# Kernel tuning notes

Hardware: AMD Instinct MI355X
Metric: run time of the kernel (lower is better)

The kernel has to match this reference:

```python
import jax, jax.numpy as jnp
import numpy as np

N = 100_000   # nodes
E = 1_600_000 # edges
D = 128       # in_dim == hidden_dim
G = 256       # graphs in batch
X = 16        # extra_in_dim (descriptor)
L = 3         # num_layers
C = 1         # n_classes
LN_EPS = 1e-5

def layer_norm(x, gamma, beta):
    mu = jnp.mean(x, axis=-1, keepdims=True)
    var = jnp.mean(jnp.square(x - mu), axis=-1, keepdims=True)
    return (x - mu) * jax.lax.rsqrt(var + LN_EPS) * gamma + beta

def setup_inputs() -> dict:
    key = jax.random.key(0)
    ks = jax.random.split(key, 24)
    s = 0.05
    inp = {
        "h": jax.random.normal(ks[0], (N, D), dtype=jnp.float32),
        "desc": jax.random.normal(ks[1], (G, X), dtype=jnp.float32),
        "src": jax.random.randint(ks[2], (E,), 0, N, dtype=jnp.int32),
        "dst": jax.random.randint(ks[3], (E,), 0, N, dtype=jnp.int32),
        "gid": jnp.sort(jax.random.randint(ks[4], (N,), 0, G, dtype=jnp.int32)),
        # stacked per-layer GIN params (all layers D->D)
        "W1": jax.random.normal(ks[5], (L, D, D), dtype=jnp.float32) * s,
        "b1": jnp.zeros((L, D), dtype=jnp.float32),
        "g1": jnp.ones((L, D), dtype=jnp.float32),   # inner LN gamma
        "be1": jnp.zeros((L, D), dtype=jnp.float32),  # inner LN beta
        "W2": jax.random.normal(ks[6], (L, D, D), dtype=jnp.float32) * s,
        "b2": jnp.zeros((L, D), dtype=jnp.float32),
        "eps": jnp.zeros((L,), dtype=jnp.float32),    # learnable eps per layer
        "ng": jnp.ones((L, D), dtype=jnp.float32),    # outer LN gamma
        "nb": jnp.zeros((L, D), dtype=jnp.float32),   # outer LN beta
        "fc1W": jax.random.normal(ks[7], (D + X, D), dtype=jnp.float32) * s,
        "fc1b": jnp.zeros((D,), dtype=jnp.float32),
        "n1g": jnp.ones((D,), dtype=jnp.float32),
        "n1b": jnp.zeros((D,), dtype=jnp.float32),
        "fc2W": jax.random.normal(ks[8], (D, C), dtype=jnp.float32) * s,
        "fc2b": jnp.zeros((C,), dtype=jnp.float32),
    }
    return inp

def reference(h, desc, src, dst, gid, W1, b1, g1, be1, W2, b2, eps, ng, nb,
              fc1W, fc1b, n1g, n1b, fc2W, fc2b):
    for l in range(L):
        # GIN aggregation: (1+eps)*h_v + sum_{u in N(v)} h_u
        agg = jax.ops.segment_sum(h[src], dst, num_segments=N)  # [N, D]
        x = (1.0 + eps[l]) * h + agg
        # apply_func MLP: Linear -> LN -> ReLU -> (Dropout=id) -> Linear
        x = jax.nn.relu(layer_norm(x @ W1[l] + b1[l], g1[l], be1[l]))
        x = x @ W2[l] + b2[l]
        # outer norm + relu (dropout = identity at eval)
        h = jax.nn.relu(layer_norm(x, ng[l], nb[l]))
    hg = jax.ops.segment_sum(h, gid, num_segments=G)  # sum pooling [G, D]
    x = jnp.concatenate([hg, desc], axis=1)           # [G, D+X]
    x = jax.nn.relu(layer_norm(x @ fc1W + fc1b, n1g, n1b))
    return x @ fc2W + fc2b                            # [G, C]
```

## Files before the change

### kernel.cpp

```cpp
#include <hip/hip_runtime.h>

#define NN 100000
#define NE 1600000
#define DD 128
#define NG 256
#define XX 16
#define NL 3
#define NBK 391
#define LNEPS 1e-5f

typedef _Float16 half8 __attribute__((ext_vector_type(8)));
typedef _Float16 half4v __attribute__((ext_vector_type(4)));
typedef float f32x4 __attribute__((ext_vector_type(4)));

__global__ __launch_bounds__(256) void hist_k(const int* __restrict__ dst,
                                              int* __restrict__ hist) {
    __shared__ int lh[NBK];
    const int t = threadIdx.x, blk = blockIdx.x;
    for (int i = t; i < NBK; i += 256) lh[i] = 0;
    __syncthreads();
    const int base = blk * (NE / 256);
    for (int e = base + t; e < base + NE / 256; e += 256)
        atomicAdd(&lh[dst[e] >> 8], 1);
    __syncthreads();
    for (int i = t; i < NBK; i += 256) hist[i * 256 + blk] = lh[i];
}

__global__ __launch_bounds__(256) void bucketpref_k(int* __restrict__ hist,
                                                    int* __restrict__ btot) {
    __shared__ int sd[256];
    const int b = blockIdx.x, t = threadIdx.x;
    int v = hist[b * 256 + t];
    sd[t] = v;
    __syncthreads();
    #pragma unroll
    for (int off = 1; off < 256; off <<= 1) {
        int x = t >= off ? sd[t - off] : 0;
        __syncthreads();
        sd[t] += x;
        __syncthreads();
    }
    hist[b * 256 + t] = sd[t] - v;
    if (t == 255) btot[b] = sd[255];
}

__global__ __launch_bounds__(512) void scan_bsums2_k(int* __restrict__ bsum, int nb,
                                                     int* __restrict__ row_ptr) {
    __shared__ int sd[512];
    int t = threadIdx.x;
    int v = t < nb ? bsum[t] : 0;
    sd[t] = v;
    __syncthreads();
    #pragma unroll
    for (int off = 1; off < 512; off <<= 1) {
        int x = t >= off ? sd[t - off] : 0;
        __syncthreads();
        sd[t] += x;
        __syncthreads();
    }
    if (t < nb) bsum[t] = sd[t] - v;
    if (t == 0) row_ptr[NN] = NE;
}

__global__ __launch_bounds__(256) void scatter_pairs_k(const int* __restrict__ src,
                                                       const int* __restrict__ dst,
                                                       const int* __restrict__ btot,
                                                       const int* __restrict__ hist,
                                                       unsigned* __restrict__ pairs) {
    __shared__ int off[NBK];
    const int t = threadIdx.x, blk = blockIdx.x;
    for (int i = t; i < NBK; i += 256)
        off[i] = btot[i] + hist[i * 256 + blk];
    __syncthreads();
    const int base = blk * (NE / 256);
    for (int e = base + t; e < base + NE / 256; e += 256) {
        int d = dst[e];
        int pos = atomicAdd(&off[d >> 8], 1);
        pairs[pos] = ((unsigned)(d & 255) << 17) | (unsigned)src[e];
    }
}

__global__ __launch_bounds__(256) void bucket_csr_k(const unsigned* __restrict__ pairs,
                                                    const int* __restrict__ btot,
                                                    int* __restrict__ row_ptr,
                                                    int* __restrict__ col) {
    __shared__ int cntL[256], ex[256], rnk[256], sd[256];
    const int b = blockIdx.x, t = threadIdx.x;
    const int nbase = b << 8;
    const int ps = btot[b];
    const int pe = (b == NBK - 1) ? NE : btot[b + 1];
    cntL[t] = 0; rnk[t] = 0;
    __syncthreads();
    for (int i = ps + t; i < pe; i += 256)
        atomicAdd(&cntL[pairs[i] >> 17], 1);
    __syncthreads();
    int v = cntL[t];
    sd[t] = v;
    __syncthreads();
    #pragma unroll
    for (int off = 1; off < 256; off <<= 1) {
        int x = t >= off ? sd[t - off] : 0;
        __syncthreads();
        sd[t] += x;
        __syncthreads();
    }
    ex[t] = sd[t] - v;
    int node = nbase + t;
    if (node < NN) row_ptr[node] = ps + ex[t];
    __syncthreads();
    for (int i = ps + t; i < pe; i += 256) {
        unsigned p = pairs[i];
        int li = p >> 17;
        int r = atomicAdd(&rnk[li], 1);
        col[ps + ex[li] + r] = (int)(p & 0x1FFFFu);
    }
}

__global__ __launch_bounds__(256) void h16init_k(const float* __restrict__ h,
                                                 _Float16* __restrict__ h16) {
    size_t i = (size_t)blockIdx.x * 256 + threadIdx.x;
    if (i >= (size_t)NN * DD / 4) return;
    float4 v = ((const float4*)h)[i];
    half4v o;
    o.x = (_Float16)v.x; o.y = (_Float16)v.y; o.z = (_Float16)v.z; o.w = (_Float16)v.w;
    ((half4v*)h16)[i] = o;
}

__global__ __launch_bounds__(256) void agg_k(const float* __restrict__ h,
                                             const _Float16* __restrict__ h16,
                                             const int* __restrict__ row_ptr,
                                             const int* __restrict__ col,
                                             _Float16* __restrict__ xhi,
                                             _Float16* __restrict__ xlo,
                                             const float* __restrict__ eps, int l) {
    const float e = 1.0f + eps[l];
    const int v = blockIdx.x * 8 + (threadIdx.x >> 5);
    const int q = threadIdx.x & 31;
    if (v >= NN) return;
    const int lo = row_ptr[v], hi = row_ptr[v + 1];
    float4 a0 = *(const float4*)&h[(size_t)v * DD + q * 4];
    a0.x *= e; a0.y *= e; a0.z *= e; a0.w *= e;
    float4 a1 = make_float4(0.f, 0.f, 0.f, 0.f);
    float4 a2 = make_float4(0.f, 0.f, 0.f, 0.f);
    float4 a3 = make_float4(0.f, 0.f, 0.f, 0.f);
    int i = lo;
    for (; i + 8 <= hi; i += 8) {
        int s0 = col[i],     s1 = col[i + 1], s2 = col[i + 2], s3 = col[i + 3];
        int s4 = col[i + 4], s5 = col[i + 5], s6 = col[i + 6], s7 = col[i + 7];
        half4v g0 = *(const half4v*)&h16[(size_t)s0 * DD + q * 4];
        half4v g1 = *(const half4v*)&h16[(size_t)s1 * DD + q * 4];
        half4v g2 = *(const half4v*)&h16[(size_t)s2 * DD + q * 4];
        half4v g3 = *(const half4v*)&h16[(size_t)s3 * DD + q * 4];
        half4v g4 = *(const half4v*)&h16[(size_t)s4 * DD + q * 4];
        half4v g5 = *(const half4v*)&h16[(size_t)s5 * DD + q * 4];
        half4v g6 = *(const half4v*)&h16[(size_t)s6 * DD + q * 4];
        half4v g7 = *(const half4v*)&h16[(size_t)s7 * DD + q * 4];
        a0.x += (float)g0.x + (float)g4.x; a0.y += (float)g0.y + (float)g4.y;
        a0.z += (float)g0.z + (float)g4.z; a0.w += (float)g0.w + (float)g4.w;
        a1.x += (float)g1.x + (float)g5.x; a1.y += (float)g1.y + (float)g5.y;
        a1.z += (float)g1.z + (float)g5.z; a1.w += (float)g1.w + (float)g5.w;
        a2.x += (float)g2.x + (float)g6.x; a2.y += (float)g2.y + (float)g6.y;
        a2.z += (float)g2.z + (float)g6.z; a2.w += (float)g2.w + (float)g6.w;
        a3.x += (float)g3.x + (float)g7.x; a3.y += (float)g3.y + (float)g7.y;
        a3.z += (float)g3.z + (float)g7.z; a3.w += (float)g3.w + (float)g7.w;
    }
    for (; i + 2 <= hi; i += 2) {
        int s0 = col[i], s1 = col[i + 1];
        half4v g0 = *(const half4v*)&h16[(size_t)s0 * DD + q * 4];
        half4v g1 = *(const half4v*)&h16[(size_t)s1 * DD + q * 4];
        a0.x += (float)g0.x; a0.y += (float)g0.y; a0.z += (float)g0.z; a0.w += (float)g0.w;
        a1.x += (float)g1.x; a1.y += (float)g1.y; a1.z += (float)g1.z; a1.w += (float)g1.w;
    }
    if (i < hi) {
        int s = col[i];
        half4v g = *(const half4v*)&h16[(size_t)s * DD + q * 4];
        a0.x += (float)g.x; a0.y += (float)g.y; a0.z += (float)g.z; a0.w += (float)g.w;
    }
    a0.x += a1.x + a2.x + a3.x;
    a0.y += a1.y + a2.y + a3.y;
    a0.z += a1.z + a2.z + a3.z;
    a0.w += a1.w + a2.w + a3.w;
    union { _Float16 hh[4]; float2 f; } ph, pl;
    ph.hh[0] = (_Float16)a0.x; pl.hh[0] = (_Float16)((a0.x - (float)ph.hh[0]) * 2048.0f);
    ph.hh[1] = (_Float16)a0.y; pl.hh[1] = (_Float16)((a0.y - (float)ph.hh[1]) * 2048.0f);
    ph.hh[2] = (_Float16)a0.z; pl.hh[2] = (_Float16)((a0.z - (float)ph.hh[2]) * 2048.0f);
    ph.hh[3] = (_Float16)a0.w; pl.hh[3] = (_Float16)((a0.w - (float)ph.hh[3]) * 2048.0f);
    *(float2*)&xhi[(size_t)v * DD + q * 4] = ph.f;
    *(float2*)&xlo[(size_t)v * DD + q * 4] = pl.f;
}

__global__ __launch_bounds__(256) void wprep_k(const float* __restrict__ W1,
                                               const float* __restrict__ W2,
                                               _Float16* __restrict__ wt) {
    int idx = blockIdx.x * 256 + threadIdx.x;
    if (idx >= 6 * 16384) return;
    int mtx = idx >> 14;
    int r = idx & 16383;
    int c = r >> 7, k = r & 127;
    int l = mtx >> 1;
    const float* W = (mtx & 1) ? W2 : W1;
    float w = W[(size_t)l * 16384 + k * 128 + c];
    _Float16 hi = (_Float16)w;
    _Float16 lo = (_Float16)((w - (float)hi) * 2048.0f);
    wt[(size_t)mtx * 2 * 16384 + r] = hi;
    wt[(size_t)mtx * 2 * 16384 + 16384 + r] = lo;
}

#define LP2 136
__global__ __launch_bounds__(256) void gemm_mfma_k(const _Float16* __restrict__ xhi,
                                                   const _Float16* __restrict__ xlo,
                                                   const _Float16* __restrict__ wthi,
                                                   const _Float16* __restrict__ wtlo,
                                                   const float* __restrict__ bias,
                                                   const float* __restrict__ gamma,
                                                   const float* __restrict__ beta,
                                                   _Float16* __restrict__ yhi,
                                                   _Float16* __restrict__ ylo,
                                                   float* __restrict__ yf,
                                                   _Float16* __restrict__ y16,
                                                   int mode, int nrows) {
    __shared__ _Float16 Ahi[64 * LP2];
    __shared__ _Float16 Alo[64 * LP2];
    __shared__ float2 part[4][64];

    const int tid = threadIdx.x;
    const int wc = tid >> 6;
    const int lane = tid & 63;
    const int cl = lane & 15, gq = lane >> 4;
    const int rb = blockIdx.x * 64;
    const int colbase = wc * 32;

    f32x4 acc[4][2] = {};
    f32x4 acc2[4][2] = {};

    #pragma unroll
    for (int i = 0; i < 4; ++i) {
        int c = tid + 256 * i;
        int row = c >> 4, kc = c & 15;
        int gr = rb + row;
        int sr = gr < nrows ? gr : 0;
        *(float4*)&Ahi[row * LP2 + kc * 8] =
            *(const float4*)&xhi[(size_t)sr * DD + kc * 8];
        *(float4*)&Alo[row * LP2 + kc * 8] =
            *(const float4*)&xlo[(size_t)sr * DD + kc * 8];
    }
    __syncthreads();

    #pragma unroll
    for (int kt = 0; kt < 4; ++kt) {
        half8 bh[2], bl[2], ah[4], al[4];
        #pragma unroll
        for (int n = 0; n < 2; ++n) {
            int c = colbase + n * 16 + cl;
            bh[n] = *(const half8*)&wthi[(size_t)c * DD + kt * 32 + gq * 8];
            bl[n] = *(const half8*)&wtlo[(size_t)c * DD + kt * 32 + gq * 8];
        }
        #pragma unroll
        for (int m = 0; m < 4; ++m) {
            int row = m * 16 + cl;
            ah[m] = *(const half8*)&Ahi[row * LP2 + kt * 32 + gq * 8];
            al[m] = *(const half8*)&Alo[row * LP2 + kt * 32 + gq * 8];
        }
        #pragma unroll
        for (int m = 0; m < 4; ++m)
            #pragma unroll
            for (int n = 0; n < 2; ++n) {
                acc[m][n]  = __builtin_amdgcn_mfma_f32_16x16x32_f16(ah[m], bh[n], acc[m][n], 0, 0, 0);
                acc2[m][n] = __builtin_amdgcn_mfma_f32_16x16x32_f16(ah[m], bl[n], acc2[m][n], 0, 0, 0);
                acc2[m][n] = __builtin_amdgcn_mfma_f32_16x16x32_f16(al[m], bh[n], acc2[m][n], 0, 0, 0);
            }
    }

    float bv[2], gv[2], bev[2];
    #pragma unroll
    for (int n = 0; n < 2; ++n) {
        int c = colbase + n * 16 + cl;
        bv[n] = bias[c]; gv[n] = gamma[c]; bev[n] = beta[c];
    }
    #pragma unroll
    for (int m = 0; m < 4; ++m)
        #pragma unroll
        for (int j = 0; j < 4; ++j) {
            float s1 = 0.f, s2 = 0.f;
            #pragma unroll
            for (int n = 0; n < 2; ++n) {
                float z = acc[m][n][j] + acc2[m][n][j] * (1.0f / 2048.0f) + bv[n];
                acc[m][n][j] = z;
                s1 += z; s2 += z * z;
            }
            #pragma unroll
            for (int msk = 1; msk <= 8; msk <<= 1) {
                s1 += __shfl_xor(s1, msk);
                s2 += __shfl_xor(s2, msk);
            }
            if (cl == 0) part[wc][m * 16 + gq * 4 + j] = make_float2(s1, s2);
        }
    __syncthreads();
    #pragma unroll
    for (int m = 0; m < 4; ++m)
        #pragma unroll
        for (int j = 0; j < 4; ++j) {
            int r = m * 16 + gq * 4 + j;
            float2 p0 = part[0][r], p1 = part[1][r], p2 = part[2][r], p3 = part[3][r];
            float s1 = p0.x + p1.x + p2.x + p3.x;
            float s2 = p0.y + p1.y + p2.y + p3.y;
            float mean = s1 * (1.0f / DD);
            float inv = rsqrtf(s2 * (1.0f / DD) - mean * mean + LNEPS);
            int grow = rb + r;
            if (grow < nrows) {
                #pragma unroll
                for (int n = 0; n < 2; ++n) {
                    float o = fmaxf((acc[m][n][j] - mean) * inv * gv[n] + bev[n], 0.f);
                    int c = colbase + n * 16 + cl;
                    if (mode == 0) {
                        _Float16 oh = (_Float16)o;
                        _Float16 ol = (_Float16)((o - (float)oh) * 2048.0f);
                        yhi[(size_t)grow * DD + c] = oh;
                        ylo[(size_t)grow * DD + c] = ol;
                    } else {
                        yf[(size_t)grow * DD + c] = o;
                        if (y16) y16[(size_t)grow * DD + c] = (_Float16)o;
                    }
                }
            }
        }
}

__global__ __launch_bounds__(256) void zero_int_k(int* __restrict__ p, int n) {
    int i = blockIdx.x * 256 + threadIdx.x;
    if (i < n) p[i] = 0;
}

__global__ __launch_bounds__(256) void pool_k(const float* __restrict__ h,
                                              const int* __restrict__ gid,
                                              float* __restrict__ hg) {
    const int c = threadIdx.x & 127;
    const int half = threadIdx.x >> 7;
    int base = blockIdx.x * 128 + half * 64;
    if (base >= NN) return;
    int end = base + 64; if (end > NN) end = NN;
    float acc = 0.f;
    int cg = gid[base];
    for (int n = base; n < end; ++n) {
        int g = gid[n];
        if (g != cg) {
            unsafeAtomicAdd(&hg[cg * DD + c], acc);
            acc = 0.f; cg = g;
        }
        acc += h[(size_t)n * DD + c];
    }
    unsafeAtomicAdd(&hg[cg * DD + c], acc);
}

__global__ __launch_bounds__(128) void head2_k(const float* __restrict__ hg,
                                               const float* __restrict__ desc,
                                               const float* __restrict__ fc1W,
                                               const float* __restrict__ fc1b,
                                               const float* __restrict__ n1g,
                                               const float* __restrict__ n1b,
                                               const float* __restrict__ fc2W,
                                               const float* __restrict__ fc2b,
                                               float* __restrict__ out) {
    const int g = blockIdx.x;
    const int c = threadIdx.x;
    __shared__ float cat[DD + XX];
    __shared__ float red[4];
    cat[c] = hg[g * DD + c];
    if (c < XX) cat[DD + c] = desc[g * XX + c];
    __syncthreads();
    float z = fc1b[c];
    for (int k = 0; k < DD + XX; ++k) z += cat[k] * fc1W[k * DD + c];
    float s1 = z, s2 = z * z;
    #pragma unroll
    for (int m = 1; m <= 32; m <<= 1) { s1 += __shfl_xor(s1, m); s2 += __shfl_xor(s2, m); }
    int wid = c >> 6, lane = c & 63;
    if (lane == 0) { red[wid] = s1; red[2 + wid] = s2; }
    __syncthreads();
    s1 = red[0] + red[1]; s2 = red[2] + red[3];
    float mean = s1 * (1.0f / DD);
    float var  = s2 * (1.0f / DD) - mean * mean;
    float inv  = rsqrtf(var + LNEPS);
    float zr = fmaxf((z - mean) * inv * n1g[c] + n1b[c], 0.f);
    float p = zr * fc2W[c];
    #pragma unroll
    for (int m = 1; m <= 32; m <<= 1) p += __shfl_xor(p, m);
    __syncthreads();
    if (lane == 0) red[wid] = p;
    __syncthreads();
    if (c == 0) out[g] = red[0] + red[1] + fc2b[0];
}

extern "C" void kernel_launch(void* const* d_in, const int* in_sizes, int n_in,
                              void* d_out, int out_size, void* d_ws, size_t ws_size,
                              hipStream_t stream) {
    const float* h    = (const float*)d_in[0];
    const float* desc = (const float*)d_in[1];
    const int*   src  = (const int*)d_in[2];
    const int*   dst  = (const int*)d_in[3];
    const int*   gid  = (const int*)d_in[4];
    const float* W1   = (const float*)d_in[5];
    const float* b1   = (const float*)d_in[6];
    const float* g1   = (const float*)d_in[7];
    const float* be1  = (const float*)d_in[8];
    const float* W2   = (const float*)d_in[9];
    const float* b2   = (const float*)d_in[10];
    const float* eps  = (const float*)d_in[11];
    const float* ng   = (const float*)d_in[12];
    const float* nb   = (const float*)d_in[13];
    const float* fc1W = (const float*)d_in[14];
    const float* fc1b = (const float*)d_in[15];
    const float* n1g  = (const float*)d_in[16];
    const float* n1b  = (const float*)d_in[17];
    const float* fc2W = (const float*)d_in[18];
    const float* fc2b = (const float*)d_in[19];
    float* out = (float*)d_out;

    float* nx = (float*)d_ws;
    _Float16* XAhi = (_Float16*)(nx + (size_t)NN * DD);
    _Float16* XAlo = XAhi + (size_t)NN * DD;
    _Float16* h16  = XAlo + (size_t)NN * DD;
    float* hg = (float*)(h16 + (size_t)NN * DD);
    int* row_ptr = (int*)(hg + (size_t)NG * DD);
    int* col     = row_ptr + NN + 4;
    int* btot    = col + NE;
    _Float16* wt = (_Float16*)(((uintptr_t)(btot + 512) + 255) & ~(uintptr_t)255);
    unsigned* pairs = (unsigned*)XAhi;
    int*      hist  = (int*)XAlo;

    wprep_k<<<(6 * 16384 + 255) / 256, 256, 0, stream>>>(W1, W2, wt);
    h16init_k<<<(NN * DD / 4 + 255) / 256, 256, 0, stream>>>(h, h16);

    hist_k<<<256, 256, 0, stream>>>(dst, hist);
    bucketpref_k<<<NBK, 256, 0, stream>>>(hist, btot);
    scan_bsums2_k<<<1, 512, 0, stream>>>(btot, NBK, row_ptr);
    scatter_pairs_k<<<256, 256, 0, stream>>>(src, dst, btot, hist, pairs);
    bucket_csr_k<<<NBK, 256, 0, stream>>>(pairs, btot, row_ptr, col);

    const int gemm_grid = (NN + 63) / 64;
    const float* cur = h;
    for (int l = 0; l < NL; ++l) {
        const _Float16* w1hi = wt + (size_t)(l * 2 + 0) * 2 * 16384;
        const _Float16* w1lo = w1hi + 16384;
        const _Float16* w2hi = wt + (size_t)(l * 2 + 1) * 2 * 16384;
        const _Float16* w2lo = w2hi + 16384;
        agg_k<<<(NN + 7) / 8, 256, 0, stream>>>(cur, h16, row_ptr, col, XAhi, XAlo, eps, l);
        gemm_mfma_k<<<gemm_grid, 256, 0, stream>>>(
            XAhi, XAlo, w1hi, w1lo, b1 + l * DD, g1 + l * DD, be1 + l * DD,
            XAhi, XAlo, nullptr, nullptr, 0, NN);
        gemm_mfma_k<<<gemm_grid, 256, 0, stream>>>(
            XAhi, XAlo, w2hi, w2lo, b2 + l * DD, ng + l * DD, nb + l * DD,
            nullptr, nullptr, nx, (l < NL - 1) ? h16 : nullptr, 1, NN);
        cur = nx;
    }
    zero_int_k<<<(NG * DD + 255) / 256, 256, 0, stream>>>((int*)hg, NG * DD);
    pool_k<<<(NN + 127) / 128, 256, 0, stream>>>(cur, gid, hg);
    head2_k<<<NG, 128, 0, stream>>>(hg, desc, fc1W, fc1b, n1g, n1b, fc2W, fc2b, out);
}
```

Before: 714.6 us.

## Fuse both MLP GEMMs into one kernel and drop activation split-precision

The two per-layer GEMM kernels become a single kernel. The intermediate LayerNorm+ReLU output stays in shared memory as fp16 and feeds the second GEMM directly, so it no longer makes a global round trip. Activations are now stored as a single fp16 tensor instead of a hi/lo pair. This removes one write and one read of the activation buffers and one MFMA per tile, while weights keep their hi/lo split. The cost is lower precision for the aggregated sums and the hidden activations, and the histogram buffer gets its own workspace space instead of aliasing.

```diff
diff --git a/kernel.cpp b/kernel.cpp
--- a/kernel.cpp
+++ b/kernel.cpp
@@ -86,7 +86,6 @@
                                                     int* __restrict__ col) {
     __shared__ int cntL[256], ex[256], rnk[256], sd[256];
     const int b = blockIdx.x, t = threadIdx.x;
-    const int nbase = b << 8;
     const int ps = btot[b];
     const int pe = (b == NBK - 1) ? NE : btot[b + 1];
     cntL[t] = 0; rnk[t] = 0;
@@ -105,7 +104,7 @@
         __syncthreads();
     }
     ex[t] = sd[t] - v;
-    int node = nbase + t;
+    int node = (b << 8) + t;
     if (node < NN) row_ptr[node] = ps + ex[t];
     __syncthreads();
     for (int i = ps + t; i < pe; i += 256) {
@@ -130,8 +129,7 @@
                                              const _Float16* __restrict__ h16,
                                              const int* __restrict__ row_ptr,
                                              const int* __restrict__ col,
-                                             _Float16* __restrict__ xhi,
-                                             _Float16* __restrict__ xlo,
+                                             _Float16* __restrict__ x16,
                                              const float* __restrict__ eps, int l) {
     const float e = 1.0f + eps[l];
     const int v = blockIdx.x * 8 + (threadIdx.x >> 5);
@@ -180,13 +178,9 @@
     a0.y += a1.y + a2.y + a3.y;
     a0.z += a1.z + a2.z + a3.z;
     a0.w += a1.w + a2.w + a3.w;
-    union { _Float16 hh[4]; float2 f; } ph, pl;
-    ph.hh[0] = (_Float16)a0.x; pl.hh[0] = (_Float16)((a0.x - (float)ph.hh[0]) * 2048.0f);
-    ph.hh[1] = (_Float16)a0.y; pl.hh[1] = (_Float16)((a0.y - (float)ph.hh[1]) * 2048.0f);
-    ph.hh[2] = (_Float16)a0.z; pl.hh[2] = (_Float16)((a0.z - (float)ph.hh[2]) * 2048.0f);
-    ph.hh[3] = (_Float16)a0.w; pl.hh[3] = (_Float16)((a0.w - (float)ph.hh[3]) * 2048.0f);
-    *(float2*)&xhi[(size_t)v * DD + q * 4] = ph.f;
-    *(float2*)&xlo[(size_t)v * DD + q * 4] = pl.f;
+    half4v o;
+    o.x = (_Float16)a0.x; o.y = (_Float16)a0.y; o.z = (_Float16)a0.z; o.w = (_Float16)a0.w;
+    *(half4v*)&x16[(size_t)v * DD + q * 4] = o;
 }
 
 __global__ __launch_bounds__(256) void wprep_k(const float* __restrict__ W1,
@@ -207,20 +201,21 @@
 }
 
 #define LP2 136
-__global__ __launch_bounds__(256) void gemm_mfma_k(const _Float16* __restrict__ xhi,
-                                                   const _Float16* __restrict__ xlo,
-                                                   const _Float16* __restrict__ wthi,
-                                                   const _Float16* __restrict__ wtlo,
-                                                   const float* __restrict__ bias,
-                                                   const float* __restrict__ gamma,
-                                                   const float* __restrict__ beta,
-                                                   _Float16* __restrict__ yhi,
-                                                   _Float16* __restrict__ ylo,
-                                                   float* __restrict__ yf,
-                                                   _Float16* __restrict__ y16,
-                                                   int mode, int nrows) {
-    __shared__ _Float16 Ahi[64 * LP2];
-    __shared__ _Float16 Alo[64 * LP2];
+__global__ __launch_bounds__(256) void mlp_k(const _Float16* __restrict__ x16,
+                                             const _Float16* __restrict__ w1hi,
+                                             const _Float16* __restrict__ w1lo,
+                                             const _Float16* __restrict__ w2hi,
+                                             const _Float16* __restrict__ w2lo,
+                                             const float* __restrict__ b1,
+                                             const float* __restrict__ g1,
+                                             const float* __restrict__ be1,
+                                             const float* __restrict__ b2,
+                                             const float* __restrict__ ngv,
+                                             const float* __restrict__ nbv,
+                                             float* __restrict__ yf,
+                                             _Float16* __restrict__ y16,
+                                             int nrows) {
+    __shared__ _Float16 At[64 * LP2];
     __shared__ float2 part[4][64];
 
     const int tid = threadIdx.x;
@@ -230,44 +225,38 @@
     const int rb = blockIdx.x * 64;
     const int colbase = wc * 32;
 
-    f32x4 acc[4][2] = {};
-    f32x4 acc2[4][2] = {};
-
     #pragma unroll
     for (int i = 0; i < 4; ++i) {
         int c = tid + 256 * i;
         int row = c >> 4, kc = c & 15;
         int gr = rb + row;
         int sr = gr < nrows ? gr : 0;
-        *(float4*)&Ahi[row * LP2 + kc * 8] =
-            *(const float4*)&xhi[(size_t)sr * DD + kc * 8];
-        *(float4*)&Alo[row * LP2 + kc * 8] =
-            *(const float4*)&xlo[(size_t)sr * DD + kc * 8];
-    }
-    __syncthreads();
+        *(float4*)&At[row * LP2 + kc * 8] =
+            *(const float4*)&x16[(size_t)sr * DD + kc * 8];
+    }
+    __syncthreads();
+
+    f32x4 acc[4][2] = {};
+    f32x4 acc2[4][2] = {};
 
     #pragma unroll
     for (int kt = 0; kt < 4; ++kt) {
-        half8 bh[2], bl[2], ah[4], al[4];
+        half8 bh[2], bl[2], ah[4];
         #pragma unroll
         for (int n = 0; n < 2; ++n) {
             int c = colbase + n * 16 + cl;
-            bh[n] = *(const half8*)&wthi[(size_t)c * DD + kt * 32 + gq * 8];
-            bl[n] = *(const half8*)&wtlo[(size_t)c * DD + kt * 32 + gq * 8];
-        }
-        #pragma unroll
-        for (int m = 0; m < 4; ++m) {
-            int row = m * 16 + cl;
-            ah[m] = *(const half8*)&Ahi[row * LP2 + kt * 32 + gq * 8];
-            al[m] = *(const half8*)&Alo[row * LP2 + kt * 32 + gq * 8];
-        }
+            bh[n] = *(const half8*)&w1hi[(size_t)c * DD + kt * 32 + gq * 8];
+            bl[n] = *(const half8*)&w1lo[(size_t)c * DD + kt * 32 + gq * 8];
+        }
+        #pragma unroll
+        for (int m = 0; m < 4; ++m)
+            ah[m] = *(const half8*)&At[(m * 16 + cl) * LP2 + kt * 32 + gq * 8];
         #pragma unroll
         for (int m = 0; m < 4; ++m)
             #pragma unroll
             for (int n = 0; n < 2; ++n) {
                 acc[m][n]  = __builtin_amdgcn_mfma_f32_16x16x32_f16(ah[m], bh[n], acc[m][n], 0, 0, 0);
                 acc2[m][n] = __builtin_amdgcn_mfma_f32_16x16x32_f16(ah[m], bl[n], acc2[m][n], 0, 0, 0);
-                acc2[m][n] = __builtin_amdgcn_mfma_f32_16x16x32_f16(al[m], bh[n], acc2[m][n], 0, 0, 0);
             }
     }
 
@@ -275,7 +264,77 @@
     #pragma unroll
     for (int n = 0; n < 2; ++n) {
         int c = colbase + n * 16 + cl;
-        bv[n] = bias[c]; gv[n] = gamma[c]; bev[n] = beta[c];
+        bv[n] = b1[c]; gv[n] = g1[c]; bev[n] = be1[c];
+    }
+    #pragma unroll
+    for (int m = 0; m < 4; ++m)
+        #pragma unroll
+        for (int j = 0; j < 4; ++j) {
+            float s1 = 0.f, s2 = 0.f;
+            #pragma unroll
+            for (int n = 0; n < 2; ++n) {
+                float z = acc[m][n][j] + acc2[m][n][j] * (1.0f / 2048.0f) + bv[n];
+                acc[m][n][j] = z;
+                s1 += z; s2 += z * z;
+            }
+            #pragma unroll
+            for (int msk = 1; msk <= 8; msk <<= 1) {
+                s1 += __shfl_xor(s1, msk);
+                s2 += __shfl_xor(s2, msk);
+            }
+            if (cl == 0) part[wc][m * 16 + gq * 4 + j] = make_float2(s1, s2);
+        }
+    __syncthreads();
+    #pragma unroll
+    for (int m = 0; m < 4; ++m)
+        #pragma unroll
+        for (int j = 0; j < 4; ++j) {
+            int r = m * 16 + gq * 4 + j;
+            float2 p0 = part[0][r], p1 = part[1][r], p2 = part[2][r], p3 = part[3][r];
+            float s1 = p0.x + p1.x + p2.x + p3.x;
+            float s2 = p0.y + p1.y + p2.y + p3.y;
+            float mean = s1 * (1.0f / DD);
+            float inv = rsqrtf(s2 * (1.0f / DD) - mean * mean + LNEPS);
+            #pragma unroll
+            for (int n = 0; n < 2; ++n) {
+                float o = fmaxf((acc[m][n][j] - mean) * inv * gv[n] + bev[n], 0.f);
+                At[r * LP2 + colbase + n * 16 + cl] = (_Float16)o;
+            }
+        }
+    __syncthreads();
+
+    #pragma unroll
+    for (int m = 0; m < 4; ++m)
+        #pragma unroll
+        for (int n = 0; n < 2; ++n) {
+            acc[m][n]  = f32x4{0.f, 0.f, 0.f, 0.f};
+            acc2[m][n] = f32x4{0.f, 0.f, 0.f, 0.f};
+        }
+    #pragma unroll
+    for (int kt = 0; kt < 4; ++kt) {
+        half8 bh[2], bl[2], ah[4];
+        #pragma unroll
+        for (int n = 0; n < 2; ++n) {
+            int c = colbase + n * 16 + cl;
+            bh[n] = *(const half8*)&w2hi[(size_t)c * DD + kt * 32 + gq * 8];
+            bl[n] = *(const half8*)&w2lo[(size_t)c * DD + kt * 32 + gq * 8];
+        }
+        #pragma unroll
+        for (int m = 0; m < 4; ++m)
+            ah[m] = *(const half8*)&At[(m * 16 + cl) * LP2 + kt * 32 + gq * 8];
+        #pragma unroll
+        for (int m = 0; m < 4; ++m)
+            #pragma unroll
+            for (int n = 0; n < 2; ++n) {
+                acc[m][n]  = __builtin_amdgcn_mfma_f32_16x16x32_f16(ah[m], bh[n], acc[m][n], 0, 0, 0);
+                acc2[m][n] = __builtin_amdgcn_mfma_f32_16x16x32_f16(ah[m], bl[n], acc2[m][n], 0, 0, 0);
+            }
+    }
+
+    #pragma unroll
+    for (int n = 0; n < 2; ++n) {
+        int c = colbase + n * 16 + cl;
+        bv[n] = b2[c]; gv[n] = ngv[c]; bev[n] = nbv[c];
     }
     #pragma unroll
     for (int m = 0; m < 4; ++m)
@@ -312,15 +371,8 @@
                 for (int n = 0; n < 2; ++n) {
                     float o = fmaxf((acc[m][n][j] - mean) * inv * gv[n] + bev[n], 0.f);
                     int c = colbase + n * 16 + cl;
-                    if (mode == 0) {
-                        _Float16 oh = (_Float16)o;
-                        _Float16 ol = (_Float16)((o - (float)oh) * 2048.0f);
-                        yhi[(size_t)grow * DD + c] = oh;
-                        ylo[(size_t)grow * DD + c] = ol;
-                    } else {
-                        yf[(size_t)grow * DD + c] = o;
-                        if (y16) y16[(size_t)grow * DD + c] = (_Float16)o;
-                    }
+                    yf[(size_t)grow * DD + c] = o;
+                    if (y16) y16[(size_t)grow * DD + c] = (_Float16)o;
                 }
             }
         }
@@ -416,16 +468,15 @@
     float* out = (float*)d_out;
 
     float* nx = (float*)d_ws;
-    _Float16* XAhi = (_Float16*)(nx + (size_t)NN * DD);
-    _Float16* XAlo = XAhi + (size_t)NN * DD;
-    _Float16* h16  = XAlo + (size_t)NN * DD;
+    _Float16* x16 = (_Float16*)(nx + (size_t)NN * DD);
+    _Float16* h16 = x16 + (size_t)NN * DD;
     float* hg = (float*)(h16 + (size_t)NN * DD);
     int* row_ptr = (int*)(hg + (size_t)NG * DD);
     int* col     = row_ptr + NN + 4;
     int* btot    = col + NE;
-    _Float16* wt = (_Float16*)(((uintptr_t)(btot + 512) + 255) & ~(uintptr_t)255);
-    unsigned* pairs = (unsigned*)XAhi;
-    int*      hist  = (int*)XAlo;
+    int* hist    = btot + 512;
+    _Float16* wt = (_Float16*)(((uintptr_t)(hist + NBK * 256) + 255) & ~(uintptr_t)255);
+    unsigned* pairs = (unsigned*)x16;
 
     wprep_k<<<(6 * 16384 + 255) / 256, 256, 0, stream>>>(W1, W2, wt);
     h16init_k<<<(NN * DD / 4 + 255) / 256, 256, 0, stream>>>(h, h16);
@@ -436,20 +487,19 @@
     scatter_pairs_k<<<256, 256, 0, stream>>>(src, dst, btot, hist, pairs);
     bucket_csr_k<<<NBK, 256, 0, stream>>>(pairs, btot, row_ptr, col);
 
-    const int gemm_grid = (NN + 63) / 64;
+    const int mlp_grid = (NN + 63) / 64;
     const float* cur = h;
     for (int l = 0; l < NL; ++l) {
         const _Float16* w1hi = wt + (size_t)(l * 2 + 0) * 2 * 16384;
         const _Float16* w1lo = w1hi + 16384;
         const _Float16* w2hi = wt + (size_t)(l * 2 + 1) * 2 * 16384;
         const _Float16* w2lo = w2hi + 16384;
-        agg_k<<<(NN + 7) / 8, 256, 0, stream>>>(cur, h16, row_ptr, col, XAhi, XAlo, eps, l);
-        gemm_mfma_k<<<gemm_grid, 256, 0, stream>>>(
-            XAhi, XAlo, w1hi, w1lo, b1 + l * DD, g1 + l * DD, be1 + l * DD,
-            XAhi, XAlo, nullptr, nullptr, 0, NN);
-        gemm_mfma_k<<<gemm_grid, 256, 0, stream>>>(
-            XAhi, XAlo, w2hi, w2lo, b2 + l * DD, ng + l * DD, nb + l * DD,
-            nullptr, nullptr, nx, (l < NL - 1) ? h16 : nullptr, 1, NN);
+        agg_k<<<(NN + 7) / 8, 256, 0, stream>>>(cur, h16, row_ptr, col, x16, eps, l);
+        mlp_k<<<mlp_grid, 256, 0, stream>>>(
+            x16, w1hi, w1lo, w2hi, w2lo,
+            b1 + l * DD, g1 + l * DD, be1 + l * DD,
+            b2 + l * DD, ng + l * DD, nb + l * DD,
+            nx, (l < NL - 1) ? h16 : nullptr, NN);
         cur = nx;
     }
     zero_int_k<<<(NG * DD + 255) / 256, 256, 0, stream>>>((int*)hg, NG * DD);
```

After: 615.3 us. 13.9% less time.
